# Kernel optimization log

Measured on AMD Instinct MI355X. Metric: run time of the kernel, lower is better.

Reference implementation:

```python
import jax, jax.numpy as jnp
import numpy as np

B, N, NY = 2, 4096, 4096
ENC_DIM, DEC_DIM, H = 768, 512, 8
HEAD_DIM = DEC_DIM // H
SCALE = HEAD_DIM ** -0.5


def setup_inputs() -> dict:
    key = jax.random.key(0)
    ks = jax.random.split(key, 8)
    lim_q = 1.0 / np.sqrt(DEC_DIM)
    lim_kv = 1.0 / np.sqrt(ENC_DIM)
    return {
        "x": jax.random.normal(ks[0], (B, N, DEC_DIM), jnp.float32),
        "y": jax.random.normal(ks[1], (B, NY, ENC_DIM), jnp.float32),
        "key_padding_mask": jax.random.randint(ks[2], (B, NY), 0, 2).astype(bool),
        "Wq": jax.random.uniform(ks[3], (DEC_DIM, DEC_DIM), jnp.float32, -lim_q, lim_q),
        "Wkv": jax.random.uniform(ks[4], (2 * DEC_DIM, ENC_DIM), jnp.float32, -lim_kv, lim_kv),
        "Wp": jax.random.uniform(ks[5], (DEC_DIM, DEC_DIM), jnp.float32, -lim_q, lim_q),
        "bp": jax.random.uniform(ks[6], (DEC_DIM,), jnp.float32, -lim_q, lim_q),
    }


def reference(x, y, key_padding_mask, Wq, Wkv, Wp, bp):
    # q projection: [B,N,C] -> [B,H,N,D]
    q = (x @ Wq.T).reshape(B, N, H, HEAD_DIM).transpose(0, 2, 1, 3)
    # kv projection: [B,Ny,E] -> [B,Ny,2C] -> k,v each [B,H,Ny,D]
    kv = (y @ Wkv.T).reshape(B, NY, 2, H, HEAD_DIM).transpose(2, 0, 3, 1, 4)
    k, v = kv[0], kv[1]
    # attention scores [B,H,N,Ny]
    attn = jnp.einsum("bhnd,bhmd->bhnm", q, k) * SCALE
    attn = jnp.where(key_padding_mask[:, None, None, :], -jnp.inf, attn)
    attn = jax.nn.softmax(attn, axis=-1)
    out = jnp.einsum("bhnm,bhmd->bhnd", attn, v)  # [B,H,N,D]
    out = out.transpose(0, 2, 1, 3).reshape(B, N, DEC_DIM)
    return out @ Wp.T + bp
```

## Files before the change

### kernel.cpp

```cpp
#include <hip/hip_runtime.h>
#include <hip/hip_bf16.h>
#include <stdint.h>

typedef __bf16 bf16_t;
typedef __bf16 bf16x8 __attribute__((ext_vector_type(8)));
typedef __bf16 bf16x4 __attribute__((ext_vector_type(4)));
typedef float  f32x4  __attribute__((ext_vector_type(4)));

#define MFMA16(a, b, c) __builtin_amdgcn_mfma_f32_16x16x32_bf16((a), (b), (c), 0, 0, 0)

__device__ __forceinline__ void gload_lds16(const void* g, void* l) {
  __builtin_amdgcn_global_load_lds((const __attribute__((address_space(1))) void*)g,
                                   (__attribute__((address_space(3))) void*)l, 16, 0, 0);
}

#define QSCALE 0.18033688011112042f
#define NE_X   4194304UL
#define NE_Y   6291456UL
#define NE_WQ  262144UL
#define NE_WKV 786432UL
#define NE_WP  262144UL
#define NE_BP  512UL

__global__ void detect_and_mask(const uint16_t* __restrict__ xu,
                                const uint8_t* __restrict__ mk,
                                int* __restrict__ flags, bf16_t* __restrict__ mmul) {
  __shared__ int cbf, c3f1, c3f3, cnz;
  const int t = threadIdx.x;
  if (t == 0) { cbf = 0; c3f1 = 0; c3f3 = 0; cnz = 0; }
  __syncthreads();
  if (blockIdx.x == 0) {
    int local = 0;
    for (int i = t; i < 2048; i += 256) {
      uint16_t u = xu[2 * i];
      int e = (u >> 7) & 0xFF;
      if (u == 0 || (e >= 0x66 && e <= 0x88)) local++;
    }
    atomicAdd(&cbf, local);
  }
  int l1 = 0, l3 = 0, lnz = 0;
  for (int i = t; i < 4096; i += 256) {
    uint8_t b = mk[i];
    int p = i & 3;
    if (p == 1 && b == 0x3F) l1++;
    if (p == 3 && b == 0x3F) l3++;
    if (p != 0 && b != 0) lnz++;
  }
  atomicAdd(&c3f1, l1);
  atomicAdd(&c3f3, l3);
  atomicAdd(&cnz, lnz);
  __syncthreads();
  if (blockIdx.x == 0 && t == 0) flags[0] = (cbf > 1536) ? 1 : 0;
  const int fmt = (c3f1 > 0) ? 2 : (c3f3 > 0) ? 3 : (cnz > 0) ? 0 : 1;
  const int i = blockIdx.x * 256 + t;
  bool on;
  if (fmt == 0)      on = mk[i] != 0;
  else if (fmt == 1) on = ((const int*)mk)[i] != 0;
  else if (fmt == 2) on = (((const uint16_t*)mk)[i] & 0x7FFF) != 0;
  else               on = ((const float*)mk)[i] != 0.0f;
  mmul[i] = on ? (bf16_t)0.0f : (bf16_t)1.0f;
}

__global__ void convert_all(const void* __restrict__ x, const void* __restrict__ y,
                            const void* __restrict__ wq, const void* __restrict__ wkv,
                            const void* __restrict__ wp, const void* __restrict__ bp,
                            uint16_t* __restrict__ dst, const int* __restrict__ flags) {
  const size_t E0 = NE_X, E1 = E0 + NE_Y, E2 = E1 + NE_WQ, E3 = E2 + NE_WKV,
               E4 = E3 + NE_WP, E5 = E4 + NE_BP;
  size_t i8 = ((size_t)blockIdx.x * 256 + threadIdx.x) * 8;
  if (i8 >= E5) return;
  const void* src; size_t off;
  if      (i8 < E0) { src = x;   off = i8; }
  else if (i8 < E1) { src = y;   off = i8 - E0; }
  else if (i8 < E2) { src = wq;  off = i8 - E1; }
  else if (i8 < E3) { src = wkv; off = i8 - E2; }
  else if (i8 < E4) { src = wp;  off = i8 - E3; }
  else              { src = bp;  off = i8 - E4; }
  const bool isWq = (i8 >= E1 && i8 < E2);
  if (flags[0] && !isWq) {
    *(uint4*)(dst + i8) = *(const uint4*)((const uint16_t*)src + off);
    return;
  }
  float v[8];
  if (flags[0]) {
    const uint16_t* u = (const uint16_t*)src + off;
    for (int j = 0; j < 8; ++j) {
      union { uint32_t q; float f; } c; c.q = ((uint32_t)u[j]) << 16; v[j] = c.f;
    }
  } else {
    const float* f = (const float*)src + off;
    float4 a = *(const float4*)f;
    float4 b2 = *(const float4*)(f + 4);
    v[0] = a.x; v[1] = a.y; v[2] = a.z; v[3] = a.w;
    v[4] = b2.x; v[5] = b2.y; v[6] = b2.z; v[7] = b2.w;
  }
  const float sc = isWq ? QSCALE : 1.0f;
  union { bf16_t h[8]; uint4 u; } pk;
  for (int j = 0; j < 8; ++j) pk.h[j] = (bf16_t)(v[j] * sc);
  *(uint4*)(dst + i8) = pk.u;
}

template <int K, int MODE>
__launch_bounds__(256, 2)
__global__ void gemm_bt(const bf16_t* __restrict__ A, const bf16_t* __restrict__ W,
                        const bf16_t* __restrict__ bias, void* __restrict__ C,
                        bf16_t* __restrict__ Vt, const int* __restrict__ flags, int Ncols) {
  __shared__ __align__(16) char lds[32768];
  const int t = threadIdx.x;
  const int w = t >> 6, lane = t & 63, quad = lane >> 4, l16 = lane & 15;
  const int wr = w >> 1, wc = w & 1;
  const int m0 = blockIdx.y * 128, n0 = blockIdx.x * 128;

  f32x4 acc[4][4] = {};
  const int rowS = t >> 2, uS = t & 3;
  constexpr int NK = K / 32;

  auto stage = [&](int ks, int buf) {
    char* ldsA = lds + buf * 16384;
    char* ldsW = ldsA + 8192;
    const int k0 = ks * 32;
    for (int i = 0; i < 2; ++i) {
      int row = i * 64 + rowS;
      int c = uS ^ ((row >> 1) & 3);
      gload_lds16(A + (size_t)(m0 + row) * K + k0 + c * 8, ldsA + i * 4096 + w * 1024);
      gload_lds16(W + (size_t)(n0 + row) * K + k0 + c * 8, ldsW + i * 4096 + w * 1024);
    }
  };

  stage(0, 0);
  for (int ks = 0; ks < NK; ++ks) {
    const int cur = ks & 1;
    if (ks + 1 < NK) {
      stage(ks + 1, cur ^ 1);
      asm volatile("s_waitcnt vmcnt(4)" ::: "memory");
    } else {
      asm volatile("s_waitcnt vmcnt(0)" ::: "memory");
    }
    __builtin_amdgcn_sched_barrier(0);
    __builtin_amdgcn_s_barrier();
    const char* ldsA = lds + cur * 16384;
    const char* ldsW = ldsA + 8192;
    bf16x8 af[4], bfr[4];
    for (int mt = 0; mt < 4; ++mt) {
      int row = wr * 64 + mt * 16 + l16;
      int us = quad ^ ((row >> 1) & 3);
      af[mt] = *(const bf16x8*)(ldsA + row * 64 + us * 16);
    }
    for (int nt = 0; nt < 4; ++nt) {
      int row = wc * 64 + nt * 16 + l16;
      int us = quad ^ ((row >> 1) & 3);
      bfr[nt] = *(const bf16x8*)(ldsW + row * 64 + us * 16);
    }
    for (int mt = 0; mt < 4; ++mt)
      for (int nt = 0; nt < 4; ++nt)
        acc[mt][nt] = MFMA16(af[mt], bfr[nt], acc[mt][nt]);
    __builtin_amdgcn_s_barrier();
  }

  const int mbase = m0 + wr * 64;
  for (int nt = 0; nt < 4; ++nt) {
    const int col = n0 + wc * 64 + nt * 16 + l16;
    if (MODE == 1 && col >= 512) {
      const int hd = col - 512;
      const int hh = hd >> 6, d = hd & 63;
      const int dt = d >> 4, l15 = d & 15;
      for (int mt = 0; mt < 4; ++mt) {
        int m = mbase + mt * 16 + quad * 4;
        int bb = m >> 12, keyg = m & 4095;
        int kt = keyg >> 6, keyin = keyg & 63;
        int kc = (keyin >> 5) & 1, jq = (keyin >> 3) & 3, j0 = keyin & 7;
        const bf16_t* mmp = bias + bb * 4096 + keyg;
        union { bf16_t h4[4]; uint2 u; } pk;
        for (int r = 0; r < 4; ++r) pk.h4[r] = (bf16_t)(acc[mt][nt][r] * (float)mmp[r]);
        size_t base = (((size_t)(bb * 8 + hh) * 64 + kt) * 8 + dt * 2 + kc) * 1024
                      + (jq * 16 + l15) * 16 + j0 * 2;
        *(uint2*)((char*)Vt + base) = pk.u;
      }
    } else if (MODE == 1) {
      for (int mt = 0; mt < 4; ++mt) {
        int m = mbase + mt * 16 + quad * 4;
        for (int r = 0; r < 4; ++r)
          ((bf16_t*)C)[(size_t)(m + r) * 512 + col] = (bf16_t)acc[mt][nt][r];
      }
    } else if (MODE == 0) {
      for (int mt = 0; mt < 4; ++mt) {
        int m = mbase + mt * 16 + quad * 4;
        for (int r = 0; r < 4; ++r)
          ((bf16_t*)C)[(size_t)(m + r) * Ncols + col] = (bf16_t)acc[mt][nt][r];
      }
    } else {
      const float bv = (float)bias[col];
      const bool obf = (flags[0] != 0);
      for (int mt = 0; mt < 4; ++mt) {
        int m = mbase + mt * 16 + quad * 4;
        for (int r = 0; r < 4; ++r) {
          float v = acc[mt][nt][r] + bv;
          if (obf) ((bf16_t*)C)[(size_t)(m + r) * Ncols + col] = (bf16_t)v;
          else     ((float*)C)[(size_t)(m + r) * Ncols + col] = v;
        }
      }
    }
  }
}

__launch_bounds__(512, 2)
__global__ void attn(const bf16_t* __restrict__ Qb, const bf16_t* __restrict__ Kb,
                     const bf16_t* __restrict__ Vfb, const bf16_t* __restrict__ mmul,
                     bf16_t* __restrict__ Ob) {
  const int t = threadIdx.x, w = t >> 6, lane = t & 63, quad = lane >> 4, l16 = lane & 15;
  const int bid = blockIdx.x;
  const int h = bid & 7;
  const int b = (bid >> 3) & 1;
  const int q0 = (bid >> 4) * 256;

  __shared__ __align__(16) char lds[114688];
  char* Pw = lds + 81920 + w * 4096;
  char* Qs = lds + 49152;

  const bf16_t* Kbase = Kb + (size_t)(b * 4096) * 512 + h * 64;
  const char* Vfbase = (const char*)Vfb + (size_t)(b * 8 + h) * 524288;

  const int srow = t >> 3;
  const int sc8 = t & 7;

  auto stage_tile = [&](int kt, int slot) {
    int c = sc8 ^ (srow & 7);
    gload_lds16(Kbase + (size_t)(kt * 64 + srow) * 512 + c * 8,
                lds + slot * 8192 + w * 1024);
  };

  for (int kt = 0; kt < 6; ++kt) stage_tile(kt, kt);
  for (int i = 0; i < 4; ++i) {
    int row = i * 64 + srow;
    int c = sc8 ^ (row & 7);
    gload_lds16(Qb + (size_t)(b * 4096 + q0 + row) * 512 + h * 64 + c * 8,
                Qs + i * 8192 + w * 1024);
  }
  asm volatile("s_waitcnt vmcnt(0)" ::: "memory");
  __builtin_amdgcn_sched_barrier(0);
  __builtin_amdgcn_s_barrier();

  bf16x8 qf[2][2];
  for (int ng = 0; ng < 2; ++ng)
    for (int kc = 0; kc < 2; ++kc) {
      int row = 32 * w + 16 * ng + l16;
      int u = (4 * kc + quad) ^ (l16 & 7);
      qf[ng][kc] = *(const bf16x8*)(Qs + row * 128 + u * 16);
    }
  asm volatile("s_waitcnt lgkmcnt(0)" ::: "memory");
  __builtin_amdgcn_sched_barrier(0);
  __builtin_amdgcn_s_barrier();
  stage_tile(6, 6);
  stage_tile(7, 7);

  f32x4 o[2][4] = {};
  f32x4 lacc[2] = {};
  const int u0 = quad ^ (l16 & 7), u1 = (4 + quad) ^ (l16 & 7);

  auto process = [&](int kt, int slot) {
    const int kt0 = kt * 64;
    bf16x8 mf0 = *(const bf16x8*)(mmul + b * 4096 + kt0 + quad * 8);
    bf16x8 mf1 = *(const bf16x8*)(mmul + b * 4096 + kt0 + 32 + quad * 8);
    const char* Vtile = Vfbase + (size_t)kt * 8192;
    bf16x8 vf[4][2];
    for (int dt = 0; dt < 4; ++dt)
      for (int kc = 0; kc < 2; ++kc)
        vf[dt][kc] = *(const bf16x8*)(Vtile + (dt * 2 + kc) * 1024 + lane * 16);
    const char* Kl = lds + slot * 8192;
    bf16x8 kf[4][2];
    for (int mt = 0; mt < 4; ++mt) {
      kf[mt][0] = *(const bf16x8*)(Kl + (mt * 16 + l16) * 128 + u0 * 16);
      kf[mt][1] = *(const bf16x8*)(Kl + (mt * 16 + l16) * 128 + u1 * 16);
    }
    f32x4 z[2][4];
    __builtin_amdgcn_s_setprio(1);
    for (int ng = 0; ng < 2; ++ng)
      for (int mt = 0; mt < 4; ++mt) {
        f32x4 zz = {};
        zz = MFMA16(kf[mt][0], qf[ng][0], zz);
        z[ng][mt] = MFMA16(kf[mt][1], qf[ng][1], zz);
      }
    __builtin_amdgcn_s_setprio(0);
    for (int ng = 0; ng < 2; ++ng) {
      char* Pn = Pw + ng * 2048;
      for (int mt = 0; mt < 4; ++mt) {
        bf16x4 pk;
        pk.x = (bf16_t)__builtin_amdgcn_exp2f(z[ng][mt][0]);
        pk.y = (bf16_t)__builtin_amdgcn_exp2f(z[ng][mt][1]);
        pk.z = (bf16_t)__builtin_amdgcn_exp2f(z[ng][mt][2]);
        pk.w = (bf16_t)__builtin_amdgcn_exp2f(z[ng][mt][3]);
        int c2 = (2 * mt + (quad >> 1)) ^ (l16 & 7);
        *(bf16x4*)(Pn + l16 * 128 + c2 * 16 + (quad & 1) * 8) = pk;
      }
      bf16x8 pf0 = *(const bf16x8*)(Pn + l16 * 128 + u0 * 16);
      bf16x8 pf1 = *(const bf16x8*)(Pn + l16 * 128 + u1 * 16);
      __builtin_amdgcn_s_setprio(1);
      lacc[ng] = MFMA16(pf0, mf0, lacc[ng]);
      lacc[ng] = MFMA16(pf1, mf1, lacc[ng]);
      for (int dt = 0; dt < 4; ++dt) {
        o[ng][dt] = MFMA16(pf0, vf[dt][0], o[ng][dt]);
        o[ng][dt] = MFMA16(pf1, vf[dt][1], o[ng][dt]);
      }
      __builtin_amdgcn_s_setprio(0);
    }
  };

  int sA = 0, sB = 1;
  for (int pg = 0; pg < 32; ++pg) {
    if (pg < 29) { asm volatile("s_waitcnt vmcnt(6)" ::: "memory"); }
    else         { asm volatile("s_waitcnt vmcnt(0)" ::: "memory"); }
    __builtin_amdgcn_sched_barrier(0);
    __builtin_amdgcn_s_barrier();
    const int ktA = pg * 2;
    process(ktA, sA);
    process(ktA + 1, sB);
    if (ktA + 8 < 64) {
      int s8A = sA + 8; if (s8A >= 10) s8A -= 10;
      int s8B = sB + 8; if (s8B >= 10) s8B -= 10;
      stage_tile(ktA + 8, s8A);
      stage_tile(ktA + 9, s8B);
    }
    __builtin_amdgcn_s_barrier();
    sA += 2; if (sA >= 10) sA -= 10;
    sB += 2; if (sB >= 10) sB -= 10;
  }

  for (int ng = 0; ng < 2; ++ng) {
    float inv[4];
    for (int r = 0; r < 4; ++r) inv[r] = 1.0f / lacc[ng][r];
    for (int dt = 0; dt < 4; ++dt)
      for (int r = 0; r < 4; ++r) {
        int q = q0 + 32 * w + 16 * ng + quad * 4 + r;
        int col = h * 64 + dt * 16 + l16;
        Ob[(size_t)(b * 4096 + q) * 512 + col] = (bf16_t)(o[ng][dt][r] * inv[r]);
      }
  }
}

extern "C" void kernel_launch(void* const* d_in, const int* in_sizes, int n_in,
                              void* d_out, int out_size, void* d_ws, size_t ws_size,
                              hipStream_t stream) {
  const void* x   = d_in[0];
  const void* y   = d_in[1];
  const void* msk = d_in[2];
  const void* Wq  = d_in[3];
  const void* Wkv = d_in[4];
  const void* Wp  = d_in[5];
  const void* bp  = d_in[6];

  char* ws = (char*)d_ws;
  bf16_t* Xb   = (bf16_t*)(ws + 0);
  bf16_t* Yb   = (bf16_t*)(ws + 8388608);
  bf16_t* Wqb  = (bf16_t*)(ws + 20971520);
  bf16_t* Wkvb = (bf16_t*)(ws + 21495808);
  bf16_t* Wpb  = (bf16_t*)(ws + 23068672);
  bf16_t* bpb  = (bf16_t*)(ws + 23592960);
  bf16_t* mmul = (bf16_t*)(ws + 23593984);
  int*    flags = (int*)(ws + 23610368);
  bf16_t* Kbuf  = (bf16_t*)(ws + 25165824);
  bf16_t* Vfrag = (bf16_t*)(ws + 33554432);
  bf16_t* Qbuf  = (bf16_t*)(ws + 8388608);
  bf16_t* Obuf  = (bf16_t*)(ws + 0);

  hipLaunchKernelGGL(detect_and_mask, dim3(32), dim3(256), 0, stream,
                     (const uint16_t*)x, (const uint8_t*)msk, flags, mmul);
  hipLaunchKernelGGL(convert_all, dim3(5761), dim3(256), 0, stream,
                     x, y, Wq, Wkv, Wp, bp, (uint16_t*)ws, flags);
  hipLaunchKernelGGL((gemm_bt<768, 1>), dim3(8, 64), dim3(256), 0, stream,
                     Yb, Wkvb, mmul, (void*)Kbuf, Vfrag, flags, 1024);
  hipLaunchKernelGGL((gemm_bt<512, 0>), dim3(4, 64), dim3(256), 0, stream,
                     Xb, Wqb, (const bf16_t*)nullptr, (void*)Qbuf, (bf16_t*)nullptr, flags, 512);
  hipLaunchKernelGGL(attn, dim3(256), dim3(512), 0, stream,
                     Qbuf, Kbuf, Vfrag, mmul, Obuf);
  hipLaunchKernelGGL((gemm_bt<512, 2>), dim3(4, 64), dim3(256), 0, stream,
                     Obuf, Wpb, bpb, d_out, (bf16_t*)nullptr, flags, 512);
}
```

Measured before the change: 231.9 us.

## Merge detect/convert kernels and fuse KV and Q projection GEMMs into one launch

```diff
diff --git a/kernel.cpp b/kernel.cpp
--- a/kernel.cpp
+++ b/kernel.cpp
@@ -22,52 +22,64 @@
 #define NE_WP  262144UL
 #define NE_BP  512UL
 
-__global__ void detect_and_mask(const uint16_t* __restrict__ xu,
-                                const uint8_t* __restrict__ mk,
-                                int* __restrict__ flags, bf16_t* __restrict__ mmul) {
-  __shared__ int cbf, c3f1, c3f3, cnz;
+__global__ void prep_all(const void* __restrict__ x, const void* __restrict__ y,
+                         const void* __restrict__ wq, const void* __restrict__ wkv,
+                         const void* __restrict__ wp, const void* __restrict__ bp,
+                         const uint8_t* __restrict__ mk,
+                         uint16_t* __restrict__ dst, int* __restrict__ flags,
+                         bf16_t* __restrict__ mmul) {
   const int t = threadIdx.x;
-  if (t == 0) { cbf = 0; c3f1 = 0; c3f3 = 0; cnz = 0; }
+  const int bid = blockIdx.x;
+
+  __shared__ int cbf;
+  if (t == 0) cbf = 0;
   __syncthreads();
-  if (blockIdx.x == 0) {
+  {
+    const uint16_t* xu = (const uint16_t*)x;
     int local = 0;
-    for (int i = t; i < 2048; i += 256) {
+    for (int j = 0; j < 8; ++j) {
+      int i = t * 8 + j;
       uint16_t u = xu[2 * i];
       int e = (u >> 7) & 0xFF;
       if (u == 0 || (e >= 0x66 && e <= 0x88)) local++;
     }
     atomicAdd(&cbf, local);
   }
-  int l1 = 0, l3 = 0, lnz = 0;
-  for (int i = t; i < 4096; i += 256) {
-    uint8_t b = mk[i];
-    int p = i & 3;
-    if (p == 1 && b == 0x3F) l1++;
-    if (p == 3 && b == 0x3F) l3++;
-    if (p != 0 && b != 0) lnz++;
-  }
-  atomicAdd(&c3f1, l1);
-  atomicAdd(&c3f3, l3);
-  atomicAdd(&cnz, lnz);
   __syncthreads();
-  if (blockIdx.x == 0 && t == 0) flags[0] = (cbf > 1536) ? 1 : 0;
-  const int fmt = (c3f1 > 0) ? 2 : (c3f3 > 0) ? 3 : (cnz > 0) ? 0 : 1;
-  const int i = blockIdx.x * 256 + t;
-  bool on;
-  if (fmt == 0)      on = mk[i] != 0;
-  else if (fmt == 1) on = ((const int*)mk)[i] != 0;
-  else if (fmt == 2) on = (((const uint16_t*)mk)[i] & 0x7FFF) != 0;
-  else               on = ((const float*)mk)[i] != 0.0f;
-  mmul[i] = on ? (bf16_t)0.0f : (bf16_t)1.0f;
-}
-
-__global__ void convert_all(const void* __restrict__ x, const void* __restrict__ y,
-                            const void* __restrict__ wq, const void* __restrict__ wkv,
-                            const void* __restrict__ wp, const void* __restrict__ bp,
-                            uint16_t* __restrict__ dst, const int* __restrict__ flags) {
+  const bool isbf = (cbf > 1536);
+
+  if (bid >= 5761) {
+    const int mb = bid - 5761;
+    __shared__ int c3f1, c3f3, cnz;
+    if (t == 0) { c3f1 = 0; c3f3 = 0; cnz = 0; }
+    __syncthreads();
+    int l1 = 0, l3 = 0, lnz = 0;
+    for (int i = t; i < 4096; i += 256) {
+      uint8_t bb = mk[i];
+      int p = i & 3;
+      if (p == 1 && bb == 0x3F) l1++;
+      if (p == 3 && bb == 0x3F) l3++;
+      if (p != 0 && bb != 0) lnz++;
+    }
+    atomicAdd(&c3f1, l1);
+    atomicAdd(&c3f3, l3);
+    atomicAdd(&cnz, lnz);
+    __syncthreads();
+    if (mb == 0 && t == 0) flags[0] = isbf ? 1 : 0;
+    const int fmt = (c3f1 > 0) ? 2 : (c3f3 > 0) ? 3 : (cnz > 0) ? 0 : 1;
+    const int i = mb * 256 + t;
+    bool on;
+    if (fmt == 0)      on = mk[i] != 0;
+    else if (fmt == 1) on = ((const int*)mk)[i] != 0;
+    else if (fmt == 2) on = (((const uint16_t*)mk)[i] & 0x7FFF) != 0;
+    else               on = ((const float*)mk)[i] != 0.0f;
+    mmul[i] = on ? (bf16_t)0.0f : (bf16_t)1.0f;
+    return;
+  }
+
   const size_t E0 = NE_X, E1 = E0 + NE_Y, E2 = E1 + NE_WQ, E3 = E2 + NE_WKV,
                E4 = E3 + NE_WP, E5 = E4 + NE_BP;
-  size_t i8 = ((size_t)blockIdx.x * 256 + threadIdx.x) * 8;
+  size_t i8 = ((size_t)bid * 256 + t) * 8;
   if (i8 >= E5) return;
   const void* src; size_t off;
   if      (i8 < E0) { src = x;   off = i8; }
@@ -77,12 +89,12 @@
   else if (i8 < E4) { src = wp;  off = i8 - E3; }
   else              { src = bp;  off = i8 - E4; }
   const bool isWq = (i8 >= E1 && i8 < E2);
-  if (flags[0] && !isWq) {
+  if (isbf && !isWq) {
     *(uint4*)(dst + i8) = *(const uint4*)((const uint16_t*)src + off);
     return;
   }
   float v[8];
-  if (flags[0]) {
+  if (isbf) {
     const uint16_t* u = (const uint16_t*)src + off;
     for (int j = 0; j < 8; ++j) {
       union { uint32_t q; float f; } c; c.q = ((uint32_t)u[j]) << 16; v[j] = c.f;
@@ -101,15 +113,17 @@
 }
 
 template <int K, int MODE>
-__launch_bounds__(256, 2)
-__global__ void gemm_bt(const bf16_t* __restrict__ A, const bf16_t* __restrict__ W,
-                        const bf16_t* __restrict__ bias, void* __restrict__ C,
-                        bf16_t* __restrict__ Vt, const int* __restrict__ flags, int Ncols) {
-  __shared__ __align__(16) char lds[32768];
+__device__ __forceinline__ void gemm_core(const bf16_t* __restrict__ A,
+                                          const bf16_t* __restrict__ W,
+                                          const bf16_t* __restrict__ bias,
+                                          void* __restrict__ C,
+                                          bf16_t* __restrict__ Vt,
+                                          const int* __restrict__ flags,
+                                          int Ncols, int bx, int by, char* lds) {
   const int t = threadIdx.x;
   const int w = t >> 6, lane = t & 63, quad = lane >> 4, l16 = lane & 15;
   const int wr = w >> 1, wc = w & 1;
-  const int m0 = blockIdx.y * 128, n0 = blockIdx.x * 128;
+  const int m0 = by * 128, n0 = bx * 128;
 
   f32x4 acc[4][4] = {};
   const int rowS = t >> 2, uS = t & 3;
@@ -201,6 +215,33 @@
       }
     }
   }
+}
+
+__launch_bounds__(256, 2)
+__global__ void gemm_kvq(const bf16_t* __restrict__ Yb, const bf16_t* __restrict__ Wkvb,
+                         const bf16_t* __restrict__ mmul, bf16_t* __restrict__ Kbuf,
+                         bf16_t* __restrict__ Vfrag,
+                         const bf16_t* __restrict__ Xb, const bf16_t* __restrict__ Wqb,
+                         bf16_t* __restrict__ Qbuf, const int* __restrict__ flags) {
+  __shared__ __align__(16) char lds[32768];
+  const int bid = blockIdx.x;
+  if (bid < 512) {
+    gemm_core<768, 1>(Yb, Wkvb, mmul, (void*)Kbuf, Vfrag, flags, 1024,
+                      bid & 7, bid >> 3, lds);
+  } else {
+    const int q = bid - 512;
+    gemm_core<512, 0>(Xb, Wqb, nullptr, (void*)Qbuf, nullptr, flags, 512,
+                      q & 3, q >> 2, lds);
+  }
+}
+
+__launch_bounds__(256, 2)
+__global__ void gemm_out(const bf16_t* __restrict__ A, const bf16_t* __restrict__ W,
+                         const bf16_t* __restrict__ bias, void* __restrict__ C,
+                         const int* __restrict__ flags) {
+  __shared__ __align__(16) char lds[32768];
+  gemm_core<512, 2>(A, W, bias, C, nullptr, flags, 512,
+                    blockIdx.x, blockIdx.y, lds);
 }
 
 __launch_bounds__(512, 2)
@@ -362,16 +403,13 @@
   bf16_t* Qbuf  = (bf16_t*)(ws + 8388608);
   bf16_t* Obuf  = (bf16_t*)(ws + 0);
 
-  hipLaunchKernelGGL(detect_and_mask, dim3(32), dim3(256), 0, stream,
-                     (const uint16_t*)x, (const uint8_t*)msk, flags, mmul);
-  hipLaunchKernelGGL(convert_all, dim3(5761), dim3(256), 0, stream,
-                     x, y, Wq, Wkv, Wp, bp, (uint16_t*)ws, flags);
-  hipLaunchKernelGGL((gemm_bt<768, 1>), dim3(8, 64), dim3(256), 0, stream,
-                     Yb, Wkvb, mmul, (void*)Kbuf, Vfrag, flags, 1024);
-  hipLaunchKernelGGL((gemm_bt<512, 0>), dim3(4, 64), dim3(256), 0, stream,
-                     Xb, Wqb, (const bf16_t*)nullptr, (void*)Qbuf, (bf16_t*)nullptr, flags, 512);
+  hipLaunchKernelGGL(prep_all, dim3(5793), dim3(256), 0, stream,
+                     x, y, Wq, Wkv, Wp, bp, (const uint8_t*)msk,
+                     (uint16_t*)ws, flags, mmul);
+  hipLaunchKernelGGL(gemm_kvq, dim3(768), dim3(256), 0, stream,
+                     Yb, Wkvb, mmul, Kbuf, Vfrag, Xb, Wqb, Qbuf, flags);
   hipLaunchKernelGGL(attn, dim3(256), dim3(512), 0, stream,
                      Qbuf, Kbuf, Vfrag, mmul, Obuf);
-  hipLaunchKernelGGL((gemm_bt<512, 2>), dim3(4, 64), dim3(256), 0, stream,
-                     Obuf, Wpb, bpb, d_out, (bf16_t*)nullptr, flags, 512);
-}
+  hipLaunchKernelGGL(gemm_out, dim3(4, 64), dim3(256), 0, stream,
+                     Obuf, Wpb, bpb, d_out, flags);
+}
```

Result: slower. 244.6 us (+5.5%).
